# Kernel tuning notes

Measured on AMD Instinct MI355X. Metric: run time of the kernel, lower is better.

Reference implementation:

```python
import jax, jax.numpy as jnp
import numpy as np

HID = 1024
HEADS = 16
DH = HID // HEADS
SCALE = DH ** -0.5
L, B = 2048, 2


def setup_inputs() -> dict:
    key = jax.random.key(0)
    ks = jax.random.split(key, 16)
    inp = {
        "query": jax.random.normal(ks[0], (L, B, HID), jnp.float32),
        "key": jax.random.normal(ks[1], (L, B, HID), jnp.float32),
        "value": jax.random.normal(ks[2], (L, B, HID), jnp.float32),
        "mask": jax.random.randint(ks[3], (B, L), 0, 2).astype(bool),
    }
    # xavier-uniform linear weights (torch Linear stores [out, in]; y = x @ W.T + b)
    lim = (6.0 / (HID + HID)) ** 0.5
    for i, name in enumerate(["wq", "wk", "wv", "wfc"]):
        inp[name] = jax.random.uniform(ks[4 + i], (HID, HID), jnp.float32, -lim, lim)
    inp["bq"] = jnp.zeros((HID,), jnp.float32)
    inp["bk"] = jnp.zeros((HID,), jnp.float32)
    inp["bv"] = jnp.zeros((HID,), jnp.float32)
    inp["bfc"] = jnp.zeros((HID,), jnp.float32)
    inp["tao"] = jnp.full((HEADS,), 10.0, jnp.float32)
    return inp


def reference(query, key, value, mask, wq, bq, wk, bk, wv, bv, wfc, bfc, tao):
    # inputs arrive [L, B, D]; module transposes to [B, L, D]
    q = jnp.swapaxes(query, 0, 1)
    k = jnp.swapaxes(key, 0, 1)
    v = jnp.swapaxes(value, 0, 1)
    bsz, length, _ = q.shape

    def heads(x, w, b):
        y = x @ w.T + b                      # [B, L, D]
        return y.reshape(bsz, length, HEADS, DH).transpose(0, 2, 1, 3)  # [B, H, L, d]

    Q = heads(q, wq, bq)
    K = heads(k, wk, bk)
    V = heads(v, wv, bv)

    qk = jnp.einsum("bhqd,bhkd->bhqk", Q, K) * SCALE  # [B, H, L, L]

    # gaussian positional bias: -|i-j|^2/2 * tao_h^-4
    idx = jnp.arange(length, dtype=jnp.float32)
    dist = -0.5 * (idx[:, None] - idx[None, :]) ** 2          # [L, L]
    qk = qk + dist[None, None, :, :] * (tao ** -4)[None, :, None, None]

    qk = jnp.where(mask[:, None, None, :], -jnp.inf, qk)
    attn = jax.nn.softmax(qk, axis=-1)  # dropout is identity in eval mode

    x = jnp.einsum("bhqk,bhkd->bhqd", attn, V)            # [B, H, L, d]
    x = x.transpose(0, 2, 1, 3).reshape(bsz, length, HID)  # [B, L, D]
    x = x @ wfc.T + bfc
    return jnp.swapaxes(x, 0, 1)  # [L, B, D]
```

## Files before the change

### kernel.cpp

```cpp
#include <hip/hip_runtime.h>

#define LQ   2048
#define BQ   2
#define HID  1024
#define NH   16
#define DH   64
#define SCALE 0.125f
#define L2E  1.44269504088896f
#define C1   0.18033688011f
#define EXPOFF 23.0831206542f

using short8  = __attribute__((ext_vector_type(8))) short;
using ushort8 = __attribute__((ext_vector_type(8))) unsigned short;
using f32x4   = __attribute__((ext_vector_type(4))) float;
typedef unsigned short u16;
typedef __attribute__((ext_vector_type(2))) __bf16 bf16x2;

__device__ inline u16 f2bf(float x) {
    unsigned int u = __float_as_uint(x);
    u = (u + 0x7fffu + ((u >> 16) & 1u)) >> 16;
    return (u16)u;
}

#if defined(__has_builtin)
#if __has_builtin(__builtin_amdgcn_cvt_pk_bf16_f32)
#define HAVE_PKBF 1
#endif
#if __has_builtin(__builtin_amdgcn_exp2f)
#define HAVE_EXP2 1
#endif
#endif

__device__ inline unsigned int pkbf(float a, float b) {
#ifdef HAVE_PKBF
    bf16x2 r = __builtin_amdgcn_cvt_pk_bf16_f32(a, b);
    return __builtin_bit_cast(unsigned int, r);
#else
    return (unsigned int)f2bf(a) | ((unsigned int)f2bf(b) << 16);
#endif
}

__device__ inline float fexp2(float x) {
#ifdef HAVE_EXP2
    return __builtin_amdgcn_exp2f(x);
#else
    return exp2f(x);
#endif
}

__device__ inline void gl_lds16(const void* g, void* l) {
    __builtin_amdgcn_global_load_lds(
        (const __attribute__((address_space(1))) void*)g,
        (__attribute__((address_space(3))) void*)l, 16, 0, 0);
}

struct CastArgs {
    const float* s[7];
    u16* d[7];
    int n[7];
    const unsigned char* mraw;
    int* mout;
    int mn;
};

__global__ __launch_bounds__(256) void castw(CastArgs a) {
    const int y = blockIdx.y;
    const int t = threadIdx.x;
    if (y == 7) {
        if (blockIdx.x != 0) return;
        __shared__ int cnt;
        if (t == 0) cnt = 0;
        __syncthreads();
        int local = 0;
        for (int i = t; i < a.mn; i += 256)
            if ((i & 3) && a.mraw[i]) local++;
        atomicAdd(&cnt, local);
        __syncthreads();
        bool isInt32 = (cnt == 0);
        const int* mi = (const int*)a.mraw;
        for (int i = t; i < a.mn; i += 256)
            a.mout[i] = isInt32 ? mi[i] : (int)a.mraw[i];
        return;
    }
    const float* s = a.s[y];
    u16* d = a.d[y];
    const int n4 = a.n[y] >> 2;
    for (int i = blockIdx.x * 256 + t; i < n4; i += gridDim.x * 256) {
        float4 v = *(const float4*)(s + (size_t)i * 4);
        uint2 p;
        p.x = pkbf(v.x, v.y);
        p.y = pkbf(v.z, v.w);
        *(uint2*)(d + (size_t)i * 4) = p;
    }
}

struct QkvArgs {
    const u16* A[3];
    const u16* W[3];
    const float* bias[3];
    u16* out[3];
};

__global__ __launch_bounds__(256) void gemm_qkv(QkvArgs ga) {
    __shared__ u16 As[2][128][64];
    __shared__ u16 Bs[2][128][64];

    const int z = blockIdx.z;
    const u16* A = ga.A[z];
    const u16* W = ga.W[z];
    const float* bias = ga.bias[z];
    u16* outp = ga.out[z];

    const int t = threadIdx.x;
    const int m0 = blockIdx.x * 128;
    const int n0 = blockIdx.y * 128;
    const int lane = t & 63;
    const int lane15 = lane & 15;
    const int quad = lane >> 4;
    const int w = t >> 6;
    const int wm = (w >> 1) * 64;
    const int wn = (w & 1) * 64;

    const int lrow = lane >> 3;
    const int ch = (lane & 7) ^ ((lane >> 3) & 7);
    const u16* aS = A + (size_t)(m0 + 32 * w + lrow) * HID + 8 * ch;
    const u16* bS = W + (size_t)(n0 + 32 * w + lrow) * HID + 8 * ch;

    const int s0 = (quad ^ (lane15 & 7)) * 8;
    const int s1 = ((4 + quad) ^ (lane15 & 7)) * 8;

    f32x4 acc[4][4];
#pragma unroll
    for (int i = 0; i < 4; i++)
#pragma unroll
        for (int j = 0; j < 4; j++) acc[i][j] = (f32x4){0,0,0,0};

#pragma unroll
    for (int i = 0; i < 4; i++) {
        gl_lds16(aS + (size_t)(8 * i) * HID, &As[0][32 * w + 8 * i][0]);
        gl_lds16(bS + (size_t)(8 * i) * HID, &Bs[0][32 * w + 8 * i][0]);
    }
    __syncthreads();

    int p = 0;
    for (int k0 = 0; k0 < HID; k0 += 64) {
        short8 af0[4], af1[4], bf0[4], bf1[4];
#pragma unroll
        for (int i = 0; i < 4; i++) {
            const u16* ar = &As[p][wm + i * 16 + lane15][0];
            const u16* br = &Bs[p][wn + i * 16 + lane15][0];
            af0[i] = *(const short8*)(ar + s0);
            af1[i] = *(const short8*)(ar + s1);
            bf0[i] = *(const short8*)(br + s0);
            bf1[i] = *(const short8*)(br + s1);
        }
        if (k0 + 64 < HID) {
#pragma unroll
            for (int i = 0; i < 4; i++) {
                gl_lds16(aS + (size_t)(8 * i) * HID + (k0 + 64), &As[p ^ 1][32 * w + 8 * i][0]);
                gl_lds16(bS + (size_t)(8 * i) * HID + (k0 + 64), &Bs[p ^ 1][32 * w + 8 * i][0]);
            }
        }
#pragma unroll
        for (int mi = 0; mi < 4; mi++)
#pragma unroll
            for (int ni = 0; ni < 4; ni++) {
                acc[mi][ni] = __builtin_amdgcn_mfma_f32_16x16x32_bf16(af0[mi], bf0[ni], acc[mi][ni], 0, 0, 0);
                acc[mi][ni] = __builtin_amdgcn_mfma_f32_16x16x32_bf16(af1[mi], bf1[ni], acc[mi][ni], 0, 0, 0);
            }
        __syncthreads();
        p ^= 1;
    }

#pragma unroll
    for (int mi = 0; mi < 4; mi++) {
#pragma unroll
        for (int ni = 0; ni < 4; ni++) {
            const int n = n0 + wn + ni * 16 + lane15;
            const float bv = bias[n];
            const int h = n >> 6, d = n & 63;
#pragma unroll
            for (int r = 0; r < 4; r++) {
                const int m = m0 + wm + mi * 16 + quad * 4 + r;
                const float c = acc[mi][ni][r] + bv;
                const int b = m & 1, l = m >> 1;
                if (z < 2) {
                    outp[(((size_t)(b * NH + h)) * LQ + l) * DH + d] = f2bf(c);
                } else {
                    outp[(((size_t)(b * NH + h)) * DH + d) * LQ + l] = f2bf(c);
                }
            }
        }
    }
}

__global__ __launch_bounds__(256) void gemm_fc(const u16* __restrict__ A,
                                               const u16* __restrict__ W,
                                               const float* __restrict__ bias,
                                               float* __restrict__ outp) {
    __shared__ u16 As[2][128][64];
    __shared__ u16 Bs[2][64][64];

    const int t = threadIdx.x;
    const int m0 = blockIdx.x * 128;
    const int n0 = blockIdx.y * 64;
    const int lane = t & 63;
    const int lane15 = lane & 15;
    const int quad = lane >> 4;
    const int w = t >> 6;
    const int wm = (w >> 1) * 64;
    const int wn = (w & 1) * 32;

    const int lrow = lane >> 3;
    const int ch = (lane & 7) ^ ((lane >> 3) & 7);
    const u16* aS = A + (size_t)(m0 + 32 * w + lrow) * HID + 8 * ch;
    const u16* bS = W + (size_t)(n0 + 16 * w + lrow) * HID + 8 * ch;

    const int s0 = (quad ^ (lane15 & 7)) * 8;
    const int s1 = ((4 + quad) ^ (lane15 & 7)) * 8;

    f32x4 acc[4][2];
#pragma unroll
    for (int i = 0; i < 4; i++)
#pragma unroll
        for (int j = 0; j < 2; j++) acc[i][j] = (f32x4){0,0,0,0};

#pragma unroll
    for (int i = 0; i < 4; i++)
        gl_lds16(aS + (size_t)(8 * i) * HID, &As[0][32 * w + 8 * i][0]);
#pragma unroll
    for (int i = 0; i < 2; i++)
        gl_lds16(bS + (size_t)(8 * i) * HID, &Bs[0][16 * w + 8 * i][0]);
    __syncthreads();

    int p = 0;
    for (int k0 = 0; k0 < HID; k0 += 64) {
        short8 af0[4], af1[4], bf0[2], bf1[2];
#pragma unroll
        for (int i = 0; i < 4; i++) {
            const u16* ar = &As[p][wm + i * 16 + lane15][0];
            af0[i] = *(const short8*)(ar + s0);
            af1[i] = *(const short8*)(ar + s1);
        }
#pragma unroll
        for (int j = 0; j < 2; j++) {
            const u16* br = &Bs[p][wn + j * 16 + lane15][0];
            bf0[j] = *(const short8*)(br + s0);
            bf1[j] = *(const short8*)(br + s1);
        }
        if (k0 + 64 < HID) {
#pragma unroll
            for (int i = 0; i < 4; i++)
                gl_lds16(aS + (size_t)(8 * i) * HID + (k0 + 64), &As[p ^ 1][32 * w + 8 * i][0]);
#pragma unroll
            for (int i = 0; i < 2; i++)
                gl_lds16(bS + (size_t)(8 * i) * HID + (k0 + 64), &Bs[p ^ 1][16 * w + 8 * i][0]);
        }
#pragma unroll
        for (int mi = 0; mi < 4; mi++)
#pragma unroll
            for (int ni = 0; ni < 2; ni++) {
                acc[mi][ni] = __builtin_amdgcn_mfma_f32_16x16x32_bf16(af0[mi], bf0[ni], acc[mi][ni], 0, 0, 0);
                acc[mi][ni] = __builtin_amdgcn_mfma_f32_16x16x32_bf16(af1[mi], bf1[ni], acc[mi][ni], 0, 0, 0);
            }
        __syncthreads();
        p ^= 1;
    }

#pragma unroll
    for (int mi = 0; mi < 4; mi++) {
#pragma unroll
        for (int ni = 0; ni < 2; ni++) {
            const int n = n0 + wn + ni * 16 + lane15;
            const float bv = bias[n];
#pragma unroll
            for (int r = 0; r < 4; r++) {
                const int m = m0 + wm + mi * 16 + quad * 4 + r;
                outp[(size_t)m * HID + n] = acc[mi][ni][r] + bv;
            }
        }
    }
}

#define PSTR 72

__global__ __launch_bounds__(512) void attn_kernel(const u16* __restrict__ Qg,
                                                   const u16* __restrict__ Kg,
                                                   const u16* __restrict__ Vtg,
                                                   const int* __restrict__ maskI,
                                                   const float* __restrict__ tao,
                                                   u16* __restrict__ Xa) {
    __shared__ u16 Ks[128][64];
    __shared__ u16 Vt[64][128];
    __shared__ u16 PT[128][PSTR];
    __shared__ float smask[128];

    const int bh = blockIdx.x;
    const int q0 = blockIdx.y * 128;
    const int b = bh >> 4;
    const int h = bh & 15;
    const int t = threadIdx.x;
    const int w = t >> 6;
    const int lane = t & 63;
    const int lane15 = lane & 15;
    const int quad = lane >> 4;

    const u16* Kbase = Kg + (size_t)bh * LQ * DH;
    const u16* Vtbase = Vtg + (size_t)bh * DH * LQ;
    const int* mrow = maskI + b * LQ;

    const float tv = tao[h];
    const float t2 = tv * tv;
    const float nb = -0.5f / (t2 * t2);
    const float nb2 = nb * L2E;
    const float skipd2 = -40.0f / nb2;

    const int qrow = q0 + w * 16 + lane15;
    short8 qB0, qB1;
    {
        const u16* qp_ = Qg + ((size_t)bh * LQ + qrow) * DH + quad * 8;
        qB0 = *(const short8*)(qp_);
        qB1 = *(const short8*)(qp_ + 32);
    }

    const int krow = 8 * w + (lane >> 3);
    const int kch = (lane & 7) ^ ((lane >> 3) & 7);
    const u16* kS = Kbase + (size_t)krow * DH + 8 * kch;
    const int vrow = 4 * w + (lane >> 4);
    const int vch = (lane & 8) | ((lane & 7) ^ (vrow & 7));
    const u16* vS = Vtbase + (size_t)vrow * LQ + 8 * vch;
    u16* kD0 = &Ks[8 * w][0];
    u16* kD1 = &Ks[64 + 8 * w][0];
    u16* vD0 = &Vt[4 * w][0];
    u16* vD1 = &Vt[32 + 4 * w][0];

    const int s0 = (quad ^ (lane15 & 7)) * 8;
    const int s1 = ((4 + quad) ^ (lane15 & 7)) * 8;

    f32x4 O[4];
#pragma unroll
    for (int mt = 0; mt < 4; mt++) O[mt] = (f32x4){0,0,0,0};
    float l_ = 0.0f;

    const float ebase0 = (float)(qrow - quad * 4);
    const int prow = w * 16 + lane15;

    for (int k0 = 0; k0 < LQ; k0 += 128) {
        {
            int dmin = 0;
            if (k0 > q0 + 127) dmin = k0 - (q0 + 127);
            else if (k0 + 127 < q0) dmin = q0 - (k0 + 127);
            const float df = (float)dmin;
            if (df * df > skipd2) continue;
        }
        __syncthreads();
        gl_lds16(kS + (size_t)k0 * DH, kD0);
        gl_lds16(kS + (size_t)(k0 + 64) * DH, kD1);
        gl_lds16(vS + k0, vD0);
        gl_lds16(vS + (size_t)32 * LQ + k0, vD1);
        if (t < 128) smask[t] = mrow[k0 + t] ? -3.0e38f : -EXPOFF;
        __syncthreads();

#pragma unroll
        for (int hh = 0; hh < 2; hh++) {
            const int kbase = 64 * hh;
            f32x4 S[4];
#pragma unroll
            for (int kt = 0; kt < 4; kt++) {
                const u16* kr = &Ks[kbase + kt * 16 + lane15][0];
                const short8 ka = *(const short8*)(kr + s0);
                const short8 kb = *(const short8*)(kr + s1);
                S[kt] = __builtin_amdgcn_mfma_f32_16x16x32_bf16(ka, qB0, (f32x4){0,0,0,0}, 0, 0, 0);
                S[kt] = __builtin_amdgcn_mfma_f32_16x16x32_bf16(kb, qB1, S[kt], 0, 0, 0);
            }

            const float ebase = ebase0 - (float)(k0 + kbase);
            float lacc = 0.0f;
#pragma unroll
            for (int kt = 0; kt < 4; kt++) {
                const float4 sm4 = *(const float4*)&smask[kbase + kt * 16 + quad * 4];
                float p[4];
#pragma unroll
                for (int r = 0; r < 4; r++) {
                    const float d = ebase - (float)(kt * 16 + r);
                    const float tb = fmaf(nb2 * d, d, ((const float*)&sm4)[r]);
                    p[r] = fexp2(fmaf(S[kt][r], C1, tb));
                    lacc += p[r];
                }
                uint2 pk2;
                pk2.x = pkbf(p[0], p[1]);
                pk2.y = pkbf(p[2], p[3]);
                *(uint2*)&PT[prow][kt * 16 + quad * 4] = pk2;
            }
            l_ += lacc;

            const short8 pB0 = *(const short8*)&PT[prow][quad * 8];
            const short8 pB1 = *(const short8*)&PT[prow][32 + quad * 8];
#pragma unroll
            for (int mt = 0; mt < 4; mt++) {
                const u16* vr = &Vt[mt * 16 + lane15][kbase];
                const short8 va = *(const short8*)(vr + s0);
                const short8 vb = *(const short8*)(vr + s1);
                O[mt] = __builtin_amdgcn_mfma_f32_16x16x32_bf16(va, pB0, O[mt], 0, 0, 0);
                O[mt] = __builtin_amdgcn_mfma_f32_16x16x32_bf16(vb, pB1, O[mt], 0, 0, 0);
            }
        }
    }

    l_ += __shfl_xor(l_, 16, 64);
    l_ += __shfl_xor(l_, 32, 64);

    {
        const float inv = 1.0f / l_;
        u16* dst = Xa + ((size_t)qrow * BQ + b) * HID + h * DH;
#pragma unroll
        for (int mt = 0; mt < 4; mt++) {
            uint2 pk2;
            pk2.x = pkbf(O[mt][0] * inv, O[mt][1] * inv);
            pk2.y = pkbf(O[mt][2] * inv, O[mt][3] * inv);
            *(uint2*)(dst + mt * 16 + quad * 4) = pk2;
        }
    }
}

extern "C" void kernel_launch(void* const* d_in, const int* in_sizes, int n_in,
                              void* d_out, int out_size, void* d_ws, size_t ws_size,
                              hipStream_t stream) {
    const float* q    = (const float*)d_in[0];
    const float* k    = (const float*)d_in[1];
    const float* v    = (const float*)d_in[2];
    const void*  mask = d_in[3];
    const float* wq   = (const float*)d_in[4];
    const float* wk   = (const float*)d_in[5];
    const float* wv   = (const float*)d_in[6];
    const float* wfc  = (const float*)d_in[7];
    const float* bq   = (const float*)d_in[8];
    const float* bk   = (const float*)d_in[9];
    const float* bv   = (const float*)d_in[10];
    const float* bfc  = (const float*)d_in[11];
    const float* tao  = (const float*)d_in[12];

    const size_t NE = (size_t)LQ * BQ * HID;
    const size_t NW = (size_t)HID * HID;
    u16* base = (u16*)d_ws;
    u16* Qp    = base;
    u16* Kp    = base + NE;
    u16* Vtp   = base + 2 * NE;
    u16* Xa    = base + 3 * NE;
    u16* qbf   = base + 4 * NE;
    u16* kbf   = base + 5 * NE;
    u16* vbf   = base + 6 * NE;
    u16* wqbf  = base + 7 * NE;
    u16* wkbf  = wqbf + NW;
    u16* wvbf  = wkbf + NW;
    u16* wfcbf = wvbf + NW;
    int* maskI = (int*)(wfcbf + NW);

    CastArgs ca;
    ca.s[0] = q;   ca.d[0] = qbf;   ca.n[0] = (int)NE;
    ca.s[1] = k;   ca.d[1] = kbf;   ca.n[1] = (int)NE;
    ca.s[2] = v;   ca.d[2] = vbf;   ca.n[2] = (int)NE;
    ca.s[3] = wq;  ca.d[3] = wqbf;  ca.n[3] = (int)NW;
    ca.s[4] = wk;  ca.d[4] = wkbf;  ca.n[4] = (int)NW;
    ca.s[5] = wv;  ca.d[5] = wvbf;  ca.n[5] = (int)NW;
    ca.s[6] = wfc; ca.d[6] = wfcbf; ca.n[6] = (int)NW;
    ca.mraw = (const unsigned char*)mask;
    ca.mout = maskI;
    ca.mn = BQ * LQ;
    castw<<<dim3(256, 8), 256, 0, stream>>>(ca);

    QkvArgs ga;
    ga.A[0] = qbf;  ga.W[0] = wqbf;  ga.bias[0] = bq;  ga.out[0] = Qp;
    ga.A[1] = kbf;  ga.W[1] = wkbf;  ga.bias[1] = bk;  ga.out[1] = Kp;
    ga.A[2] = vbf;  ga.W[2] = wvbf;  ga.bias[2] = bv;  ga.out[2] = Vtp;
    gemm_qkv<<<dim3(32, 8, 3), 256, 0, stream>>>(ga);

    attn_kernel<<<dim3(32, 16), 512, 0, stream>>>(Qp, Kp, Vtp, maskI, tao, Xa);

    gemm_fc<<<dim3(32, 16), 256, 0, stream>>>(Xa, wfcbf, bfc, (float*)d_out);
}
```

Before: 230.1 us.

## Double-buffer K/V tiles at 64-key granularity over the Gaussian window range

Splits K and V staging into two 64-key ping-pong buffers so the next tile's global-to-LDS load is issued before computing on the current one. It iterates only over the 64-key chunks inside the Gaussian bias window instead of scanning all 128-key tiles and skipping. It also preloads the whole mask row into LDS once, removing the per-tile barrier pair, and rewrites the bias as a scaled square. The cost is more LDS for the full mask, and correctness depends on the async LDS load being complete by the next barrier.

```diff
diff --git a/kernel.cpp b/kernel.cpp
--- a/kernel.cpp
+++ b/kernel.cpp
@@ -290,10 +290,10 @@
                                                    const int* __restrict__ maskI,
                                                    const float* __restrict__ tao,
                                                    u16* __restrict__ Xa) {
-    __shared__ u16 Ks[128][64];
-    __shared__ u16 Vt[64][128];
+    __shared__ u16 Ks[2][64][64];
+    __shared__ u16 Vt[2][64][64];
     __shared__ u16 PT[128][PSTR];
-    __shared__ float smask[128];
+    __shared__ float smaskF[LQ];
 
     const int bh = blockIdx.x;
     const int q0 = blockIdx.y * 128;
@@ -313,7 +313,25 @@
     const float t2 = tv * tv;
     const float nb = -0.5f / (t2 * t2);
     const float nb2 = nb * L2E;
-    const float skipd2 = -40.0f / nb2;
+    const float sqn = sqrtf(-nb2);
+    const float R = sqrtf(-40.0f / nb2) + 1.0f;
+
+    int c_lo = (int)floorf(((float)q0 - R) * (1.0f / 64.0f));
+    int c_hi = (int)floorf(((float)(q0 + 127) + R) * (1.0f / 64.0f));
+    if (c_lo < 0) c_lo = 0;
+    if (c_hi > (LQ / 64 - 1)) c_hi = LQ / 64 - 1;
+    if (c_hi < c_lo) c_hi = c_lo;
+
+    const int lr = lane >> 3;
+    const int lc = lane & 7;
+    const int sch = lc ^ lr;
+    const u16* kS = Kbase + (size_t)(8 * w + lr) * DH + 8 * sch;
+    const u16* vS = Vtbase + (size_t)(8 * w + lr) * LQ + 8 * sch;
+
+    gl_lds16(kS + (size_t)(64 * c_lo) * DH, &Ks[0][8 * w][0]);
+    gl_lds16(vS + 64 * c_lo, &Vt[0][8 * w][0]);
+    for (int i = t; i < LQ; i += 512)
+        smaskF[i] = mrow[i] ? -3.0e38f : -EXPOFF;
 
     const int qrow = q0 + w * 16 + lane15;
     short8 qB0, qB1;
@@ -323,17 +341,6 @@
         qB1 = *(const short8*)(qp_ + 32);
     }
 
-    const int krow = 8 * w + (lane >> 3);
-    const int kch = (lane & 7) ^ ((lane >> 3) & 7);
-    const u16* kS = Kbase + (size_t)krow * DH + 8 * kch;
-    const int vrow = 4 * w + (lane >> 4);
-    const int vch = (lane & 8) | ((lane & 7) ^ (vrow & 7));
-    const u16* vS = Vtbase + (size_t)vrow * LQ + 8 * vch;
-    u16* kD0 = &Ks[8 * w][0];
-    u16* kD1 = &Ks[64 + 8 * w][0];
-    u16* vD0 = &Vt[4 * w][0];
-    u16* vD1 = &Vt[32 + 4 * w][0];
-
     const int s0 = (quad ^ (lane15 & 7)) * 8;
     const int s1 = ((4 + quad) ^ (lane15 & 7)) * 8;
 
@@ -345,66 +352,58 @@
     const float ebase0 = (float)(qrow - quad * 4);
     const int prow = w * 16 + lane15;
 
-    for (int k0 = 0; k0 < LQ; k0 += 128) {
-        {
-            int dmin = 0;
-            if (k0 > q0 + 127) dmin = k0 - (q0 + 127);
-            else if (k0 + 127 < q0) dmin = q0 - (k0 + 127);
-            const float df = (float)dmin;
-            if (df * df > skipd2) continue;
-        }
+    __syncthreads();
+
+    int p = 0;
+    for (int c = c_lo; c <= c_hi; ++c) {
+        if (c < c_hi) {
+            gl_lds16(kS + (size_t)(64 * (c + 1)) * DH, &Ks[p ^ 1][8 * w][0]);
+            gl_lds16(vS + 64 * (c + 1), &Vt[p ^ 1][8 * w][0]);
+        }
+
+        f32x4 S[4];
+#pragma unroll
+        for (int kt = 0; kt < 4; kt++) {
+            const u16* kr = &Ks[p][kt * 16 + lane15][0];
+            const short8 ka = *(const short8*)(kr + s0);
+            const short8 kb = *(const short8*)(kr + s1);
+            S[kt] = __builtin_amdgcn_mfma_f32_16x16x32_bf16(ka, qB0, (f32x4){0,0,0,0}, 0, 0, 0);
+            S[kt] = __builtin_amdgcn_mfma_f32_16x16x32_bf16(kb, qB1, S[kt], 0, 0, 0);
+        }
+
+        const float eb = (ebase0 - (float)(64 * c)) * sqn;
+        float lacc = 0.0f;
+#pragma unroll
+        for (int kt = 0; kt < 4; kt++) {
+            const float4 sm4 = *(const float4*)&smaskF[64 * c + kt * 16 + quad * 4];
+            float pr[4];
+#pragma unroll
+            for (int r = 0; r < 4; r++) {
+                const float dp = eb - (float)(kt * 16 + r) * sqn;
+                const float tb = fmaf(-dp, dp, ((const float*)&sm4)[r]);
+                pr[r] = fexp2(fmaf(S[kt][r], C1, tb));
+                lacc += pr[r];
+            }
+            uint2 pk2;
+            pk2.x = pkbf(pr[0], pr[1]);
+            pk2.y = pkbf(pr[2], pr[3]);
+            *(uint2*)&PT[prow][kt * 16 + quad * 4] = pk2;
+        }
+        l_ += lacc;
+
+        const short8 pB0 = *(const short8*)&PT[prow][quad * 8];
+        const short8 pB1 = *(const short8*)&PT[prow][32 + quad * 8];
+#pragma unroll
+        for (int mt = 0; mt < 4; mt++) {
+            const u16* vr = &Vt[p][mt * 16 + lane15][0];
+            const short8 va = *(const short8*)(vr + s0);
+            const short8 vb = *(const short8*)(vr + s1);
+            O[mt] = __builtin_amdgcn_mfma_f32_16x16x32_bf16(va, pB0, O[mt], 0, 0, 0);
+            O[mt] = __builtin_amdgcn_mfma_f32_16x16x32_bf16(vb, pB1, O[mt], 0, 0, 0);
+        }
+
         __syncthreads();
-        gl_lds16(kS + (size_t)k0 * DH, kD0);
-        gl_lds16(kS + (size_t)(k0 + 64) * DH, kD1);
-        gl_lds16(vS + k0, vD0);
-        gl_lds16(vS + (size_t)32 * LQ + k0, vD1);
-        if (t < 128) smask[t] = mrow[k0 + t] ? -3.0e38f : -EXPOFF;
-        __syncthreads();
-
-#pragma unroll
-        for (int hh = 0; hh < 2; hh++) {
-            const int kbase = 64 * hh;
-            f32x4 S[4];
-#pragma unroll
-            for (int kt = 0; kt < 4; kt++) {
-                const u16* kr = &Ks[kbase + kt * 16 + lane15][0];
-                const short8 ka = *(const short8*)(kr + s0);
-                const short8 kb = *(const short8*)(kr + s1);
-                S[kt] = __builtin_amdgcn_mfma_f32_16x16x32_bf16(ka, qB0, (f32x4){0,0,0,0}, 0, 0, 0);
-                S[kt] = __builtin_amdgcn_mfma_f32_16x16x32_bf16(kb, qB1, S[kt], 0, 0, 0);
-            }
-
-            const float ebase = ebase0 - (float)(k0 + kbase);
-            float lacc = 0.0f;
-#pragma unroll
-            for (int kt = 0; kt < 4; kt++) {
-                const float4 sm4 = *(const float4*)&smask[kbase + kt * 16 + quad * 4];
-                float p[4];
-#pragma unroll
-                for (int r = 0; r < 4; r++) {
-                    const float d = ebase - (float)(kt * 16 + r);
-                    const float tb = fmaf(nb2 * d, d, ((const float*)&sm4)[r]);
-                    p[r] = fexp2(fmaf(S[kt][r], C1, tb));
-                    lacc += p[r];
-                }
-                uint2 pk2;
-                pk2.x = pkbf(p[0], p[1]);
-                pk2.y = pkbf(p[2], p[3]);
-                *(uint2*)&PT[prow][kt * 16 + quad * 4] = pk2;
-            }
-            l_ += lacc;
-
-            const short8 pB0 = *(const short8*)&PT[prow][quad * 8];
-            const short8 pB1 = *(const short8*)&PT[prow][32 + quad * 8];
-#pragma unroll
-            for (int mt = 0; mt < 4; mt++) {
-                const u16* vr = &Vt[mt * 16 + lane15][kbase];
-                const short8 va = *(const short8*)(vr + s0);
-                const short8 vb = *(const short8*)(vr + s1);
-                O[mt] = __builtin_amdgcn_mfma_f32_16x16x32_bf16(va, pB0, O[mt], 0, 0, 0);
-                O[mt] = __builtin_amdgcn_mfma_f32_16x16x32_bf16(vb, pB1, O[mt], 0, 0, 0);
-            }
-        }
+        p ^= 1;
     }
 
     l_ += __shfl_xor(l_, 16, 64);
```

After: 240.8 us. +4.7%, slower.
